# Kernel optimization log

Measured on AMD Instinct MI355X. Metric: run time of the kernel, lower is better.

Reference implementation:

```python
import jax, jax.numpy as jnp
import numpy as np

NUM_HEADS = 8
BN_EPS = 1e-5


def _conv3x3(x, w, B, N, s):
    # x: (B, N, 3*s*s). Torch loops conv2d per batch element; equivalent to one
    # conv over the flattened (B*N, 3, s, s) batch.
    xi = x.reshape(B * N, 3, s, s)
    y = jax.lax.conv_general_dilated(
        xi, w, window_strides=(1, 1), padding='SAME',
        dimension_numbers=('NCHW', 'OIHW', 'NCHW'))
    return y.reshape(B, N, 3 * s * s)


def setup_inputs() -> dict:
    key = jax.random.key(0)
    ks = jax.random.split(key, 8)
    B, N, C, s = 4, 1024, 768, 16
    H = NUM_HEADS
    q = jax.random.normal(ks[0], (B, N, C), jnp.float32)
    k = jax.random.normal(ks[1], (B, N, C), jnp.float32)
    v = jax.random.normal(ks[2], (B, N, C), jnp.float32)
    qw = jax.random.normal(ks[3], (3, 3, 3, 3), jnp.float32) * 0.1
    kw = jax.random.normal(ks[4], (3, 3, 3, 3), jnp.float32) * 0.1
    vw = jax.random.normal(ks[5], (3, 3, 3, 3), jnp.float32) * 0.1
    rw = jax.random.normal(ks[6], (H, H), jnp.float32) * 0.3  # Conv2d(H,H,1,1) weight
    rb = jnp.zeros((H,), jnp.float32)
    bn_gamma = jnp.ones((H,), jnp.float32)
    bn_beta = jnp.zeros((H,), jnp.float32)
    pw = jax.random.normal(ks[7], (C, C), jnp.float32) * 0.02
    pb = jnp.zeros((C,), jnp.float32)
    return dict(q=q, k=k, v=v, qw=qw, kw=kw, vw=vw, rw=rw, rb=rb,
                bn_gamma=bn_gamma, bn_beta=bn_beta, pw=pw, pb=pb)


def reference(q, k, v, qw, kw, vw, rw, rb, bn_gamma, bn_beta, pw, pb):
    B, N, C = q.shape
    H = NUM_HEADS
    d = C // H
    s = int(np.sqrt(C // 3))
    scale = d ** -0.5
    # conv-projected q/k/v, back to (B, N, C)
    qc = _conv3x3(q, qw, B, N, s)
    kc = _conv3x3(k, kw, B, N, s)
    vc = _conv3x3(v, vw, B, N, s)
    # split heads: (B, H, N, d)
    qh = qc.reshape(B, N, H, d).transpose(0, 2, 1, 3)
    kh = kc.reshape(B, N, H, d).transpose(0, 2, 1, 3)
    vh = vc.reshape(B, N, H, d).transpose(0, 2, 1, 3)
    attn = jax.nn.softmax(jnp.einsum('bhnd,bhmd->bhnm', qh, kh) * scale, axis=-1)
    # re-attention: 1x1 cross-head conv + BatchNorm2d(H) in eval mode
    # (running_mean=0, running_var=1); reatten_scale = 1.0
    attn = jnp.einsum('bhnm,gh->bgnm', attn, rw) + rb[None, :, None, None]
    attn = attn * (bn_gamma / jnp.sqrt(1.0 + BN_EPS))[None, :, None, None] \
           + bn_beta[None, :, None, None]
    x = jnp.einsum('bhnm,bhmd->bhnd', attn, vh)
    x = x.transpose(0, 2, 1, 3).reshape(B, N, C)
    return x @ pw.T + pb
```

## Files before the change

### kernel.cpp

```cpp
#include <hip/hip_runtime.h>
#include <hip/hip_bf16.h>
#include <math.h>

#define B 4
#define N 1024
#define C 768
#define H 8
#define D 96

typedef _Float16 half8 __attribute__((ext_vector_type(8)));
typedef _Float16 half4 __attribute__((ext_vector_type(4)));
typedef float f32x4 __attribute__((ext_vector_type(4)));

#define BN_RSQ 0.9999950000374997f
#define QK_SCALE 0.10206207261596577f

__global__ __launch_bounds__(256) void conv_tok(const float* __restrict__ x,
                                                const float* __restrict__ w,
                                                _Float16* __restrict__ out) {
    __shared__ float sx[768];
    __shared__ float sw[81];
    int t = blockIdx.x;
    const float* xt = x + (size_t)t * 768;
    int tid = threadIdx.x;
    sx[tid]       = xt[tid];
    sx[tid + 256] = xt[tid + 256];
    sx[tid + 512] = xt[tid + 512];
    if (tid < 81) sw[tid] = w[tid];
    __syncthreads();
    int i = tid >> 4, j = tid & 15;
    float acc0 = 0.f, acc1 = 0.f, acc2 = 0.f;
    #pragma unroll
    for (int c = 0; c < 3; ++c) {
        #pragma unroll
        for (int di = 0; di < 3; ++di) {
            int ii = i + di - 1;
            if (ii < 0 || ii > 15) continue;
            #pragma unroll
            for (int dj = 0; dj < 3; ++dj) {
                int jj = j + dj - 1;
                if (jj < 0 || jj > 15) continue;
                float xv = sx[c * 256 + ii * 16 + jj];
                acc0 += xv * sw[(0 * 3 + c) * 9 + di * 3 + dj];
                acc1 += xv * sw[(1 * 3 + c) * 9 + di * 3 + dj];
                acc2 += xv * sw[(2 * 3 + c) * 9 + di * 3 + dj];
            }
        }
    }
    _Float16* ot = out + (size_t)t * 768;
    ot[0 * 256 + tid] = (_Float16)acc0;
    ot[1 * 256 + tid] = (_Float16)acc1;
    ot[2 * 256 + tid] = (_Float16)acc2;
}

__global__ __launch_bounds__(256) void transpose_v(const _Float16* __restrict__ vcH,
                                                   _Float16* __restrict__ vcT) {
    __shared__ _Float16 tile[64][66];
    int n0 = blockIdx.x * 64, c0 = blockIdx.y * 64, b = blockIdx.z;
    int tid = threadIdx.x;
    for (int i = tid; i < 4096; i += 256) {
        int r = i >> 6, c = i & 63;
        tile[r][c] = vcH[((size_t)(b * N + n0 + r)) * C + c0 + c];
    }
    __syncthreads();
    for (int i = tid; i < 4096; i += 256) {
        int cr = i >> 6, nc = i & 63;
        vcT[((size_t)(b * 768 + c0 + cr)) * N + n0 + nc] = tile[nc][cr];
    }
}

__global__ __launch_bounds__(256) void vsum_row(const _Float16* __restrict__ vcT,
                                                float* __restrict__ vsum) {
    int row = blockIdx.x * 4 + (threadIdx.x >> 6);
    int lane = threadIdx.x & 63;
    const _Float16* p = vcT + (size_t)row * N;
    float s = 0.f;
    #pragma unroll
    for (int it = 0; it < 2; ++it) {
        half8 v = *(const half8*)(p + (it * 64 + lane) * 8);
        #pragma unroll
        for (int i = 0; i < 8; ++i) s += (float)v[i];
    }
    #pragma unroll
    for (int off = 1; off < 64; off <<= 1) s += __shfl_xor(s, off);
    if (lane == 0) vsum[row] = s;
}

__global__ __launch_bounds__(256) void qk_mfma(const _Float16* __restrict__ qcH,
                                               const _Float16* __restrict__ kcH,
                                               _Float16* __restrict__ expS,
                                               float* __restrict__ Lrow) {
    __shared__ __align__(16) char smem[49152];
    char* Qb = smem;
    char* Kb = smem + 24576;
    const int n0 = blockIdx.x * 128, m0 = blockIdx.y * 128, z = blockIdx.z;
    const int b = z >> 3, h = z & 7;
    const int tid = threadIdx.x;
    const _Float16* qg = qcH + ((size_t)(b * N + n0)) * C + h * D;
    const _Float16* kg = kcH + ((size_t)(b * N + m0)) * C + h * D;
    #pragma unroll
    for (int it = 0; it < 6; ++it) {
        int chunk = it * 256 + tid;
        int r = chunk / 12, cc = (chunk - r * 12) * 8;
        half8 qv = *(const half8*)(qg + (size_t)r * C + cc);
        half8 kv = *(const half8*)(kg + (size_t)r * C + cc);
        int off = ((r * 96 + cc) * 2) ^ ((r & 7) << 4);
        *(half8*)(Qb + off) = qv;
        *(half8*)(Kb + off) = kv;
    }
    __syncthreads();
    const int wid = tid >> 6, lane = tid & 63;
    const int wr = wid >> 1, wc = wid & 1;
    const int l15 = lane & 15, l4 = lane >> 4;
    f32x4 acc[4][4] = {};
    #pragma unroll
    for (int ks = 0; ks < 3; ++ks) {
        int k0 = ks * 32 + l4 * 8;
        half8 a[4], bf[4];
        #pragma unroll
        for (int fm = 0; fm < 4; ++fm) {
            int row = wr * 64 + fm * 16 + l15;
            a[fm] = *(half8*)(Qb + (((row * 96 + k0) * 2) ^ ((row & 7) << 4)));
        }
        #pragma unroll
        for (int fn = 0; fn < 4; ++fn) {
            int row = wc * 64 + fn * 16 + l15;
            bf[fn] = *(half8*)(Kb + (((row * 96 + k0) * 2) ^ ((row & 7) << 4)));
        }
        #pragma unroll
        for (int fm = 0; fm < 4; ++fm)
            #pragma unroll
            for (int fn = 0; fn < 4; ++fn)
                acc[fm][fn] = __builtin_amdgcn_mfma_f32_16x16x32_f16(a[fm], bf[fn], acc[fm][fn], 0, 0, 0);
    }
    __syncthreads();
    #pragma unroll
    for (int fm = 0; fm < 4; ++fm) {
        #pragma unroll
        for (int j = 0; j < 4; ++j) {
            int row = wr * 64 + fm * 16 + l4 * 4 + j;
            float rs = 0.f;
            #pragma unroll
            for (int fn = 0; fn < 4; ++fn) {
                float p = __expf(acc[fm][fn][j] * QK_SCALE);
                rs += p;
                int col = wc * 64 + fn * 16 + l15;
                *(_Float16*)(smem + (row * 136 + col) * 2) = (_Float16)p;
            }
            rs += __shfl_xor(rs, 1);
            rs += __shfl_xor(rs, 2);
            rs += __shfl_xor(rs, 4);
            rs += __shfl_xor(rs, 8);
            if (l15 == 0) atomicAdd(&Lrow[z * N + n0 + row], rs);
        }
    }
    __syncthreads();
    _Float16* eg = expS + ((size_t)z * N + n0) * N + m0;
    #pragma unroll
    for (int it = 0; it < 8; ++it) {
        int q2 = it * 256 + tid;
        int row = q2 >> 4, col8 = (q2 & 15) * 8;
        half8 v = *(half8*)(smem + (row * 136 + col8) * 2);
        *(half8*)(eg + (size_t)row * N + col8) = v;
    }
}

__global__ __launch_bounds__(512, 2) void pv_fused(const _Float16* __restrict__ expS,
                                                   const float* __restrict__ Lrow,
                                                   const _Float16* __restrict__ vcT,
                                                   const float* __restrict__ rw,
                                                   const float* __restrict__ gamma,
                                                   float* __restrict__ x) {
    __shared__ _Float16 AL[8 * 64 * 32];
    __shared__ float w2s[64];
    const int n0 = blockIdx.x * 64;
    const int mbase = blockIdx.y * 256;
    const int b = blockIdx.z;
    const int tid = threadIdx.x;
    if (tid < 64) {
        int g = tid >> 3, hh = tid & 7;
        w2s[tid] = gamma[g] * BN_RSQ * rw[g * 8 + hh];
    }
    const int n_t = tid >> 3;
    const int mq = (tid & 7) * 4;
    float IL[8];
    #pragma unroll
    for (int h = 0; h < 8; ++h)
        IL[h] = 1.0f / Lrow[(size_t)(b * 8 + h) * N + n0 + n_t];
    __syncthreads();
    const int wid = tid >> 6, lane = tid & 63;
    const int l15 = lane & 15, l4 = lane >> 4;
    char* ALb = (char*)AL;
    const _Float16* vgbase = vcT + (size_t)(b * 768 + wid * 96) * N;
    f32x4 acc[4][6] = {};
    for (int msub = 0; msub < 8; ++msub) {
        const int m0 = mbase + msub * 32;
        half4 sE[8];
        #pragma unroll
        for (int h = 0; h < 8; ++h)
            sE[h] = *(const half4*)(expS + ((size_t)(b * 8 + h) * N + n0 + n_t) * N + m0 + mq);
        f32x4 Pq[8];
        #pragma unroll
        for (int h = 0; h < 8; ++h) {
            #pragma unroll
            for (int i = 0; i < 4; ++i) Pq[h][i] = (float)sE[h][i] * IL[h];
        }
        __syncthreads();
        #pragma unroll
        for (int g = 0; g < 8; ++g) {
            f32x4 v = {};
            #pragma unroll
            for (int h = 0; h < 8; ++h) {
                float wv = w2s[g * 8 + h];
                #pragma unroll
                for (int i = 0; i < 4; ++i) v[i] += wv * Pq[h][i];
            }
            half4 hv;
            #pragma unroll
            for (int i = 0; i < 4; ++i) hv[i] = (_Float16)v[i];
            *(half4*)(ALb + (g * 4096 + (((n_t * 32 + mq) * 2) ^ ((n_t & 7) << 4)))) = hv;
        }
        __syncthreads();
        half8 af[4];
        #pragma unroll
        for (int fm = 0; fm < 4; ++fm) {
            int n = fm * 16 + l15;
            af[fm] = *(half8*)(ALb + wid * 4096 + (((n * 32 + l4 * 8) * 2) ^ ((n & 7) << 4)));
        }
        #pragma unroll
        for (int fn = 0; fn < 6; ++fn) {
            int d = fn * 16 + l15;
            half8 bf = *(const half8*)(vgbase + (size_t)d * N + m0 + l4 * 8);
            #pragma unroll
            for (int fm = 0; fm < 4; ++fm)
                acc[fm][fn] = __builtin_amdgcn_mfma_f32_16x16x32_f16(af[fm], bf, acc[fm][fn], 0, 0, 0);
        }
    }
    #pragma unroll
    for (int fm = 0; fm < 4; ++fm)
        #pragma unroll
        for (int fn = 0; fn < 6; ++fn)
            #pragma unroll
            for (int j = 0; j < 4; ++j) {
                int n = n0 + fm * 16 + l4 * 4 + j;
                int c = wid * 96 + fn * 16 + l15;
                atomicAdd(&x[((size_t)(b * N + n)) * C + c], acc[fm][fn][j]);
            }
}

__global__ __launch_bounds__(256) void proj_mfma(const float* __restrict__ x,
                                                 const float* __restrict__ vsum,
                                                 const float* __restrict__ pw,
                                                 const float* __restrict__ pb,
                                                 const float* __restrict__ rb,
                                                 const float* __restrict__ gamma,
                                                 const float* __restrict__ beta,
                                                 float* __restrict__ out) {
    __shared__ _Float16 sX[128 * 32];
    __shared__ _Float16 sW[96 * 32];
    const int t0 = blockIdx.x * 128, c0 = blockIdx.y * 96;
    const int b = t0 >> 10;
    const int tid = threadIdx.x;
    const int wid = tid >> 6, lane = tid & 63;
    const int wr = wid >> 1, wc = wid & 1;
    const int l15 = lane & 15, l4 = lane >> 4;
    char* Xb = (char*)sX;
    char* Wb = (char*)sW;
    f32x4 acc[4][3] = {};
    for (int k0 = 0; k0 < 768; k0 += 32) {
        __syncthreads();
        #pragma unroll
        for (int it = 0; it < 4; ++it) {
            int q = it * 256 + tid;
            int r = q >> 3, c4 = (q & 7) * 4;
            f32x4 xv = *(const f32x4*)(x + (size_t)(t0 + r) * C + k0 + c4);
            int g = (k0 + c4) / 96;
            float cg = gamma[g] * BN_RSQ * rb[g] + beta[g];
            const f32x4 vs = *(const f32x4*)(vsum + b * 768 + k0 + c4);
            half4 hv;
            #pragma unroll
            for (int i = 0; i < 4; ++i) hv[i] = (_Float16)(xv[i] + cg * vs[i]);
            *(half4*)(Xb + (((r * 32 + c4) * 2) ^ ((r & 7) << 4))) = hv;
        }
        #pragma unroll
        for (int it = 0; it < 3; ++it) {
            int q = it * 256 + tid;
            int r = q >> 3, c4 = (q & 7) * 4;
            f32x4 wv = *(const f32x4*)(pw + (size_t)(c0 + r) * C + k0 + c4);
            half4 hv;
            #pragma unroll
            for (int i = 0; i < 4; ++i) hv[i] = (_Float16)wv[i];
            *(half4*)(Wb + (((r * 32 + c4) * 2) ^ ((r & 7) << 4))) = hv;
        }
        __syncthreads();
        half8 af[4];
        #pragma unroll
        for (int fm = 0; fm < 4; ++fm) {
            int r = wr * 64 + fm * 16 + l15;
            af[fm] = *(half8*)(Xb + (((r * 32 + l4 * 8) * 2) ^ ((r & 7) << 4)));
        }
        #pragma unroll
        for (int fn = 0; fn < 3; ++fn) {
            int r = wc * 48 + fn * 16 + l15;
            half8 bf = *(half8*)(Wb + (((r * 32 + l4 * 8) * 2) ^ ((r & 7) << 4)));
            #pragma unroll
            for (int fm = 0; fm < 4; ++fm)
                acc[fm][fn] = __builtin_amdgcn_mfma_f32_16x16x32_f16(af[fm], bf, acc[fm][fn], 0, 0, 0);
        }
    }
    #pragma unroll
    for (int fm = 0; fm < 4; ++fm)
        #pragma unroll
        for (int fn = 0; fn < 3; ++fn) {
            int cc = c0 + wc * 48 + fn * 16 + l15;
            float bias = pb[cc];
            #pragma unroll
            for (int j = 0; j < 4; ++j) {
                int t = t0 + wr * 64 + fm * 16 + l4 * 4 + j;
                out[(size_t)t * C + cc] = acc[fm][fn][j] + bias;
            }
        }
}

extern "C" void kernel_launch(void* const* d_in, const int* in_sizes, int n_in,
                              void* d_out, int out_size, void* d_ws, size_t ws_size,
                              hipStream_t stream) {
    const float* q     = (const float*)d_in[0];
    const float* k     = (const float*)d_in[1];
    const float* v     = (const float*)d_in[2];
    const float* qw    = (const float*)d_in[3];
    const float* kw    = (const float*)d_in[4];
    const float* vw    = (const float*)d_in[5];
    const float* rw    = (const float*)d_in[6];
    const float* rb    = (const float*)d_in[7];
    const float* gamma = (const float*)d_in[8];
    const float* beta  = (const float*)d_in[9];
    const float* pw    = (const float*)d_in[10];
    const float* pb    = (const float*)d_in[11];
    float* out = (float*)d_out;

    char* ws = (char*)d_ws;
    _Float16* expS = (_Float16*)ws;
    float*    xacc = (float*)(ws + 67108864);
    _Float16* qcH  = (_Float16*)(ws + 79691776);
    _Float16* kcH  = (_Float16*)(ws + 85983232);
    _Float16* vcH  = (_Float16*)(ws + 92274688);
    _Float16* vcT  = (_Float16*)(ws + 98566144);
    float*    Lrow = (float*)(ws + 104857600);
    float*    vsum = (float*)(ws + 104988672);

    hipMemsetAsync(Lrow, 0, 131072, stream);
    hipMemsetAsync(xacc, 0, 12582912, stream);

    conv_tok<<<dim3(B * N), dim3(256), 0, stream>>>(q, qw, qcH);
    conv_tok<<<dim3(B * N), dim3(256), 0, stream>>>(k, kw, kcH);
    conv_tok<<<dim3(B * N), dim3(256), 0, stream>>>(v, vw, vcH);

    transpose_v<<<dim3(16, 12, B), dim3(256), 0, stream>>>(vcH, vcT);
    vsum_row<<<dim3(768), dim3(256), 0, stream>>>(vcT, vsum);

    qk_mfma<<<dim3(8, 8, 8 * B), dim3(256), 0, stream>>>(qcH, kcH, expS, Lrow);

    pv_fused<<<dim3(16, 4, B), dim3(512), 0, stream>>>(expS, Lrow, vcT, rw, gamma, xacc);

    proj_mfma<<<dim3(32, 8), dim3(256), 0, stream>>>(xacc, vsum, pw, pb, rb, gamma, beta, out);
}
```

Before: 262.4 us.

## Recompute QK^T in PV kernel instead of materializing exp scores

```diff
diff --git a/kernel.cpp b/kernel.cpp
--- a/kernel.cpp
+++ b/kernel.cpp
@@ -86,165 +86,197 @@
     if (lane == 0) vsum[row] = s;
 }
 
-__global__ __launch_bounds__(256) void qk_mfma(const _Float16* __restrict__ qcH,
-                                               const _Float16* __restrict__ kcH,
-                                               _Float16* __restrict__ expS,
-                                               float* __restrict__ Lrow) {
+__global__ __launch_bounds__(256) void lrow_mfma(const _Float16* __restrict__ qcH,
+                                                 const _Float16* __restrict__ kcH,
+                                                 float* __restrict__ Lrow) {
     __shared__ __align__(16) char smem[49152];
     char* Qb = smem;
     char* Kb = smem + 24576;
-    const int n0 = blockIdx.x * 128, m0 = blockIdx.y * 128, z = blockIdx.z;
+    const int n0 = blockIdx.x * 128, z = blockIdx.y;
     const int b = z >> 3, h = z & 7;
     const int tid = threadIdx.x;
     const _Float16* qg = qcH + ((size_t)(b * N + n0)) * C + h * D;
-    const _Float16* kg = kcH + ((size_t)(b * N + m0)) * C + h * D;
+    const _Float16* kgb = kcH + ((size_t)(b * N)) * C + h * D;
     #pragma unroll
     for (int it = 0; it < 6; ++it) {
         int chunk = it * 256 + tid;
         int r = chunk / 12, cc = (chunk - r * 12) * 8;
         half8 qv = *(const half8*)(qg + (size_t)r * C + cc);
-        half8 kv = *(const half8*)(kg + (size_t)r * C + cc);
-        int off = ((r * 96 + cc) * 2) ^ ((r & 7) << 4);
-        *(half8*)(Qb + off) = qv;
-        *(half8*)(Kb + off) = kv;
-    }
-    __syncthreads();
+        *(half8*)(Qb + (((r * 96 + cc) * 2) ^ ((r & 7) << 4))) = qv;
+    }
     const int wid = tid >> 6, lane = tid & 63;
     const int wr = wid >> 1, wc = wid & 1;
     const int l15 = lane & 15, l4 = lane >> 4;
-    f32x4 acc[4][4] = {};
-    #pragma unroll
-    for (int ks = 0; ks < 3; ++ks) {
-        int k0 = ks * 32 + l4 * 8;
-        half8 a[4], bf[4];
-        #pragma unroll
-        for (int fm = 0; fm < 4; ++fm) {
-            int row = wr * 64 + fm * 16 + l15;
-            a[fm] = *(half8*)(Qb + (((row * 96 + k0) * 2) ^ ((row & 7) << 4)));
-        }
-        #pragma unroll
-        for (int fn = 0; fn < 4; ++fn) {
-            int row = wc * 64 + fn * 16 + l15;
-            bf[fn] = *(half8*)(Kb + (((row * 96 + k0) * 2) ^ ((row & 7) << 4)));
+    float rs[4][4] = {};
+    for (int m0 = 0; m0 < 1024; m0 += 128) {
+        __syncthreads();
+        #pragma unroll
+        for (int it = 0; it < 6; ++it) {
+            int chunk = it * 256 + tid;
+            int r = chunk / 12, cc = (chunk - r * 12) * 8;
+            half8 kv = *(const half8*)(kgb + (size_t)(m0 + r) * C + cc);
+            *(half8*)(Kb + (((r * 96 + cc) * 2) ^ ((r & 7) << 4))) = kv;
+        }
+        __syncthreads();
+        f32x4 acc[4][4] = {};
+        #pragma unroll
+        for (int ks = 0; ks < 3; ++ks) {
+            int k0 = ks * 32 + l4 * 8;
+            half8 a[4], bf[4];
+            #pragma unroll
+            for (int fm = 0; fm < 4; ++fm) {
+                int row = wr * 64 + fm * 16 + l15;
+                a[fm] = *(half8*)(Qb + (((row * 96 + k0) * 2) ^ ((row & 7) << 4)));
+            }
+            #pragma unroll
+            for (int fn = 0; fn < 4; ++fn) {
+                int row = wc * 64 + fn * 16 + l15;
+                bf[fn] = *(half8*)(Kb + (((row * 96 + k0) * 2) ^ ((row & 7) << 4)));
+            }
+            #pragma unroll
+            for (int fm = 0; fm < 4; ++fm)
+                #pragma unroll
+                for (int fn = 0; fn < 4; ++fn)
+                    acc[fm][fn] = __builtin_amdgcn_mfma_f32_16x16x32_f16(a[fm], bf[fn], acc[fm][fn], 0, 0, 0);
         }
         #pragma unroll
         for (int fm = 0; fm < 4; ++fm)
             #pragma unroll
-            for (int fn = 0; fn < 4; ++fn)
-                acc[fm][fn] = __builtin_amdgcn_mfma_f32_16x16x32_f16(a[fm], bf[fn], acc[fm][fn], 0, 0, 0);
-    }
-    __syncthreads();
-    #pragma unroll
-    for (int fm = 0; fm < 4; ++fm) {
+            for (int j = 0; j < 4; ++j) {
+                float s = 0.f;
+                #pragma unroll
+                for (int fn = 0; fn < 4; ++fn)
+                    s += __expf(acc[fm][fn][j] * QK_SCALE);
+                rs[fm][j] += s;
+            }
+    }
+    #pragma unroll
+    for (int fm = 0; fm < 4; ++fm)
         #pragma unroll
         for (int j = 0; j < 4; ++j) {
-            int row = wr * 64 + fm * 16 + l4 * 4 + j;
-            float rs = 0.f;
-            #pragma unroll
-            for (int fn = 0; fn < 4; ++fn) {
-                float p = __expf(acc[fm][fn][j] * QK_SCALE);
-                rs += p;
-                int col = wc * 64 + fn * 16 + l15;
-                *(_Float16*)(smem + (row * 136 + col) * 2) = (_Float16)p;
-            }
-            rs += __shfl_xor(rs, 1);
-            rs += __shfl_xor(rs, 2);
-            rs += __shfl_xor(rs, 4);
-            rs += __shfl_xor(rs, 8);
-            if (l15 == 0) atomicAdd(&Lrow[z * N + n0 + row], rs);
-        }
-    }
-    __syncthreads();
-    _Float16* eg = expS + ((size_t)z * N + n0) * N + m0;
-    #pragma unroll
-    for (int it = 0; it < 8; ++it) {
-        int q2 = it * 256 + tid;
-        int row = q2 >> 4, col8 = (q2 & 15) * 8;
-        half8 v = *(half8*)(smem + (row * 136 + col8) * 2);
-        *(half8*)(eg + (size_t)row * N + col8) = v;
-    }
-}
-
-__global__ __launch_bounds__(512, 2) void pv_fused(const _Float16* __restrict__ expS,
-                                                   const float* __restrict__ Lrow,
-                                                   const _Float16* __restrict__ vcT,
-                                                   const float* __restrict__ rw,
-                                                   const float* __restrict__ gamma,
-                                                   float* __restrict__ x) {
-    __shared__ _Float16 AL[8 * 64 * 32];
+            float s = rs[fm][j];
+            s += __shfl_xor(s, 1);
+            s += __shfl_xor(s, 2);
+            s += __shfl_xor(s, 4);
+            s += __shfl_xor(s, 8);
+            if (l15 == 0)
+                atomicAdd(&Lrow[z * N + n0 + wr * 64 + fm * 16 + l4 * 4 + j], s);
+        }
+}
+
+__global__ __launch_bounds__(512) void mixpv(const _Float16* __restrict__ qcH,
+                                             const _Float16* __restrict__ kcH,
+                                             const _Float16* __restrict__ vcT,
+                                             const float* __restrict__ Lrow,
+                                             const float* __restrict__ rw,
+                                             const float* __restrict__ gamma,
+                                             float* __restrict__ x) {
+    __shared__ __align__(16) _Float16 P[8 * 32 * 64];
     __shared__ float w2s[64];
-    const int n0 = blockIdx.x * 64;
-    const int mbase = blockIdx.y * 256;
+    const int n0 = blockIdx.x * 32;
+    const int msbase = blockIdx.y * 512;
     const int b = blockIdx.z;
     const int tid = threadIdx.x;
     if (tid < 64) {
         int g = tid >> 3, hh = tid & 7;
         w2s[tid] = gamma[g] * BN_RSQ * rw[g * 8 + hh];
     }
-    const int n_t = tid >> 3;
-    const int mq = (tid & 7) * 4;
+    const int n_t = tid >> 4;
+    const int mq4 = (tid & 15) * 4;
     float IL[8];
     #pragma unroll
     for (int h = 0; h < 8; ++h)
         IL[h] = 1.0f / Lrow[(size_t)(b * 8 + h) * N + n0 + n_t];
-    __syncthreads();
     const int wid = tid >> 6, lane = tid & 63;
     const int l15 = lane & 15, l4 = lane >> 4;
-    char* ALb = (char*)AL;
-    const _Float16* vgbase = vcT + (size_t)(b * 768 + wid * 96) * N;
-    f32x4 acc[4][6] = {};
-    for (int msub = 0; msub < 8; ++msub) {
-        const int m0 = mbase + msub * 32;
-        half4 sE[8];
-        #pragma unroll
-        for (int h = 0; h < 8; ++h)
-            sE[h] = *(const half4*)(expS + ((size_t)(b * 8 + h) * N + n0 + n_t) * N + m0 + mq);
-        f32x4 Pq[8];
-        #pragma unroll
-        for (int h = 0; h < 8; ++h) {
-            #pragma unroll
-            for (int i = 0; i < 4; ++i) Pq[h][i] = (float)sE[h][i] * IL[h];
-        }
-        __syncthreads();
-        #pragma unroll
-        for (int g = 0; g < 8; ++g) {
-            f32x4 v = {};
+    char* Pb = (char*)P;
+    half8 q8[2][3];
+    #pragma unroll
+    for (int fm = 0; fm < 2; ++fm)
+        #pragma unroll
+        for (int ks = 0; ks < 3; ++ks)
+            q8[fm][ks] = *(const half8*)(qcH + (size_t)(b * N + n0 + fm * 16 + l15) * C
+                                         + wid * 96 + ks * 32 + l4 * 8);
+    __syncthreads();
+    f32x4 acc_u[2][6] = {};
+    for (int mt = 0; mt < 8; ++mt) {
+        const int m0 = msbase + mt * 64;
+        #pragma unroll
+        for (int fn = 0; fn < 4; ++fn) {
+            half8 kf[3];
+            #pragma unroll
+            for (int ks = 0; ks < 3; ++ks)
+                kf[ks] = *(const half8*)(kcH + (size_t)(b * N + m0 + fn * 16 + l15) * C
+                                         + wid * 96 + ks * 32 + l4 * 8);
+            f32x4 a4[2] = {};
+            #pragma unroll
+            for (int ks = 0; ks < 3; ++ks)
+                #pragma unroll
+                for (int fm = 0; fm < 2; ++fm)
+                    a4[fm] = __builtin_amdgcn_mfma_f32_16x16x32_f16(q8[fm][ks], kf[ks], a4[fm], 0, 0, 0);
+            #pragma unroll
+            for (int fm = 0; fm < 2; ++fm)
+                #pragma unroll
+                for (int j = 0; j < 4; ++j) {
+                    float p = __expf(a4[fm][j] * QK_SCALE);
+                    int n = fm * 16 + l4 * 4 + j;
+                    int m = fn * 16 + l15;
+                    *(_Float16*)(Pb + wid * 4096 + ((n * 128 + m * 2) ^ ((n & 7) << 4))) = (_Float16)p;
+                }
+        }
+        __syncthreads();
+        {
+            f32x4 vmix[8] = {};
             #pragma unroll
             for (int h = 0; h < 8; ++h) {
-                float wv = w2s[g * 8 + h];
-                #pragma unroll
-                for (int i = 0; i < 4; ++i) v[i] += wv * Pq[h][i];
-            }
-            half4 hv;
-            #pragma unroll
-            for (int i = 0; i < 4; ++i) hv[i] = (_Float16)v[i];
-            *(half4*)(ALb + (g * 4096 + (((n_t * 32 + mq) * 2) ^ ((n_t & 7) << 4)))) = hv;
-        }
-        __syncthreads();
-        half8 af[4];
-        #pragma unroll
-        for (int fm = 0; fm < 4; ++fm) {
-            int n = fm * 16 + l15;
-            af[fm] = *(half8*)(ALb + wid * 4096 + (((n * 32 + l4 * 8) * 2) ^ ((n & 7) << 4)));
-        }
-        #pragma unroll
-        for (int fn = 0; fn < 6; ++fn) {
-            int d = fn * 16 + l15;
-            half8 bf = *(const half8*)(vgbase + (size_t)d * N + m0 + l4 * 8);
-            #pragma unroll
-            for (int fm = 0; fm < 4; ++fm)
-                acc[fm][fn] = __builtin_amdgcn_mfma_f32_16x16x32_f16(af[fm], bf, acc[fm][fn], 0, 0, 0);
-        }
-    }
-    #pragma unroll
-    for (int fm = 0; fm < 4; ++fm)
-        #pragma unroll
-        for (int fn = 0; fn < 6; ++fn)
+                half4 p4 = *(half4*)(Pb + h * 4096 + ((n_t * 128 + mq4 * 2) ^ ((n_t & 7) << 4)));
+                f32x4 pq;
+                #pragma unroll
+                for (int i = 0; i < 4; ++i) pq[i] = (float)p4[i] * IL[h];
+                #pragma unroll
+                for (int g = 0; g < 8; ++g) {
+                    float wv = w2s[g * 8 + h];
+                    #pragma unroll
+                    for (int i = 0; i < 4; ++i) vmix[g][i] += wv * pq[i];
+                }
+            }
+            #pragma unroll
+            for (int g = 0; g < 8; ++g) {
+                half4 hv;
+                #pragma unroll
+                for (int i = 0; i < 4; ++i) hv[i] = (_Float16)vmix[g][i];
+                *(half4*)(Pb + g * 4096 + ((n_t * 128 + mq4 * 2) ^ ((n_t & 7) << 4))) = hv;
+            }
+        }
+        __syncthreads();
+        #pragma unroll
+        for (int ks2 = 0; ks2 < 2; ++ks2) {
+            half8 af[2];
+            #pragma unroll
+            for (int fm = 0; fm < 2; ++fm) {
+                int n = fm * 16 + l15;
+                af[fm] = *(half8*)(Pb + wid * 4096 + ((n * 128 + (ks2 * 32 + l4 * 8) * 2) ^ ((n & 7) << 4)));
+            }
+            #pragma unroll
+            for (int fn2 = 0; fn2 < 6; ++fn2) {
+                half8 vf = *(const half8*)(vcT + (size_t)(b * 768 + wid * 96 + fn2 * 16 + l15) * N
+                                           + m0 + ks2 * 32 + l4 * 8);
+                #pragma unroll
+                for (int fm = 0; fm < 2; ++fm)
+                    acc_u[fm][fn2] = __builtin_amdgcn_mfma_f32_16x16x32_f16(af[fm], vf, acc_u[fm][fn2], 0, 0, 0);
+            }
+        }
+        __syncthreads();
+    }
+    #pragma unroll
+    for (int fm = 0; fm < 2; ++fm)
+        #pragma unroll
+        for (int fn2 = 0; fn2 < 6; ++fn2)
             #pragma unroll
             for (int j = 0; j < 4; ++j) {
                 int n = n0 + fm * 16 + l4 * 4 + j;
-                int c = wid * 96 + fn * 16 + l15;
-                atomicAdd(&x[((size_t)(b * N + n)) * C + c], acc[fm][fn][j]);
+                int c = wid * 96 + fn2 * 16 + l15;
+                atomicAdd(&x[((size_t)(b * N + n)) * C + c], acc_u[fm][fn2][j]);
             }
 }
 
@@ -340,14 +372,13 @@
     float* out = (float*)d_out;
 
     char* ws = (char*)d_ws;
-    _Float16* expS = (_Float16*)ws;
-    float*    xacc = (float*)(ws + 67108864);
-    _Float16* qcH  = (_Float16*)(ws + 79691776);
-    _Float16* kcH  = (_Float16*)(ws + 85983232);
-    _Float16* vcH  = (_Float16*)(ws + 92274688);
-    _Float16* vcT  = (_Float16*)(ws + 98566144);
-    float*    Lrow = (float*)(ws + 104857600);
-    float*    vsum = (float*)(ws + 104988672);
+    float*    xacc = (float*)ws;
+    _Float16* qcH  = (_Float16*)(ws + 12582912);
+    _Float16* kcH  = (_Float16*)(ws + 18874368);
+    _Float16* vcH  = (_Float16*)(ws + 25165824);
+    _Float16* vcT  = (_Float16*)(ws + 31457280);
+    float*    Lrow = (float*)(ws + 37748736);
+    float*    vsum = (float*)(ws + 37879808);
 
     hipMemsetAsync(Lrow, 0, 131072, stream);
     hipMemsetAsync(xacc, 0, 12582912, stream);
@@ -359,9 +390,9 @@
     transpose_v<<<dim3(16, 12, B), dim3(256), 0, stream>>>(vcH, vcT);
     vsum_row<<<dim3(768), dim3(256), 0, stream>>>(vcT, vsum);
 
-    qk_mfma<<<dim3(8, 8, 8 * B), dim3(256), 0, stream>>>(qcH, kcH, expS, Lrow);
-
-    pv_fused<<<dim3(16, 4, B), dim3(512), 0, stream>>>(expS, Lrow, vcT, rw, gamma, xacc);
+    lrow_mfma<<<dim3(8, 32), dim3(256), 0, stream>>>(qcH, kcH, Lrow);
+
+    mixpv<<<dim3(32, 2, B), dim3(512), 0, stream>>>(qcH, kcH, vcT, Lrow, rw, gamma, xacc);
 
     proj_mfma<<<dim3(32, 8), dim3(256), 0, stream>>>(xacc, vsum, pw, pb, rb, gamma, beta, out);
 }
```

Measured after the change: 273.7 us. 1.04x slower.

## Rewrite PV kernel as LDS-free register head-mixing with XCD-aware tiling; merge convs

Applied to the files above, without the earlier changes.

```diff
diff --git a/kernel.cpp b/kernel.cpp
--- a/kernel.cpp
+++ b/kernel.cpp
@@ -10,14 +10,39 @@
 
 typedef _Float16 half8 __attribute__((ext_vector_type(8)));
 typedef _Float16 half4 __attribute__((ext_vector_type(4)));
+typedef _Float16 h2 __attribute__((ext_vector_type(2)));
 typedef float f32x4 __attribute__((ext_vector_type(4)));
 
 #define BN_RSQ 0.9999950000374997f
 #define QK_SCALE 0.10206207261596577f
 
-__global__ __launch_bounds__(256) void conv_tok(const float* __restrict__ x,
-                                                const float* __restrict__ w,
-                                                _Float16* __restrict__ out) {
+static __device__ __forceinline__ h2 u32_to_h2(unsigned int u) {
+    union { unsigned int u; h2 h; } c; c.u = u; return c.h;
+}
+
+__global__ __launch_bounds__(64) void w2prep(const float* __restrict__ rw,
+                                             const float* __restrict__ gamma,
+                                             unsigned int* __restrict__ w2pk) {
+    int t = threadIdx.x;
+    int g = t >> 3, h = t & 7;
+    float w = gamma[g] * BN_RSQ * rw[g * 8 + h];
+    union { _Float16 f; unsigned short s; } c; c.f = (_Float16)w;
+    w2pk[t] = (unsigned int)c.s | ((unsigned int)c.s << 16);
+}
+
+__global__ __launch_bounds__(256) void conv_all(const float* __restrict__ q,
+                                                const float* __restrict__ k,
+                                                const float* __restrict__ v,
+                                                const float* __restrict__ qw,
+                                                const float* __restrict__ kw,
+                                                const float* __restrict__ vw,
+                                                _Float16* __restrict__ qo,
+                                                _Float16* __restrict__ ko,
+                                                _Float16* __restrict__ vo) {
+    const int sel = blockIdx.y;
+    const float* x = sel == 0 ? q : sel == 1 ? k : v;
+    const float* w = sel == 0 ? qw : sel == 1 ? kw : vw;
+    _Float16* out = sel == 0 ? qo : sel == 1 ? ko : vo;
     __shared__ float sx[768];
     __shared__ float sw[81];
     int t = blockIdx.x;
@@ -165,86 +190,79 @@
     }
 }
 
-__global__ __launch_bounds__(512, 2) void pv_fused(const _Float16* __restrict__ expS,
-                                                   const float* __restrict__ Lrow,
-                                                   const _Float16* __restrict__ vcT,
-                                                   const float* __restrict__ rw,
-                                                   const float* __restrict__ gamma,
-                                                   float* __restrict__ x) {
-    __shared__ _Float16 AL[8 * 64 * 32];
-    __shared__ float w2s[64];
-    const int n0 = blockIdx.x * 64;
-    const int mbase = blockIdx.y * 256;
-    const int b = blockIdx.z;
+__global__ __launch_bounds__(256) void pv3(const _Float16* __restrict__ expS,
+                                           const float* __restrict__ Lrow,
+                                           const _Float16* __restrict__ vcT,
+                                           const unsigned int* __restrict__ w2pk,
+                                           float* __restrict__ x) {
+    const int gid = blockIdx.x;
+    const int xcd = gid & 7;
+    const int idx = gid >> 3;
+    const int bmq = xcd * 2 + (idx & 1);
+    const int b = bmq >> 2, mq = bmq & 3;
+    const int n0 = (idx >> 1) * 16;
+    const int mbase = mq * 256;
     const int tid = threadIdx.x;
-    if (tid < 64) {
-        int g = tid >> 3, hh = tid & 7;
-        w2s[tid] = gamma[g] * BN_RSQ * rw[g * 8 + hh];
-    }
-    const int n_t = tid >> 3;
-    const int mq = (tid & 7) * 4;
-    float IL[8];
-    #pragma unroll
-    for (int h = 0; h < 8; ++h)
-        IL[h] = 1.0f / Lrow[(size_t)(b * 8 + h) * N + n0 + n_t];
-    __syncthreads();
-    const int wid = tid >> 6, lane = tid & 63;
+    const int wv = tid >> 6, lane = tid & 63;
     const int l15 = lane & 15, l4 = lane >> 4;
-    char* ALb = (char*)AL;
-    const _Float16* vgbase = vcT + (size_t)(b * 768 + wid * 96) * N;
-    f32x4 acc[4][6] = {};
-    for (int msub = 0; msub < 8; ++msub) {
-        const int m0 = mbase + msub * 32;
-        half4 sE[8];
-        #pragma unroll
-        for (int h = 0; h < 8; ++h)
-            sE[h] = *(const half4*)(expS + ((size_t)(b * 8 + h) * N + n0 + n_t) * N + m0 + mq);
-        f32x4 Pq[8];
-        #pragma unroll
-        for (int h = 0; h < 8; ++h) {
-            #pragma unroll
-            for (int i = 0; i < 4; ++i) Pq[h][i] = (float)sE[h][i] * IL[h];
-        }
-        __syncthreads();
-        #pragma unroll
-        for (int g = 0; g < 8; ++g) {
-            f32x4 v = {};
+    const int g0 = wv * 2;
+    h2 IL2[8];
+    #pragma unroll
+    for (int h = 0; h < 8; ++h) {
+        float il = 1.0f / Lrow[(size_t)(b * 8 + h) * N + n0 + l15];
+        _Float16 i16 = (_Float16)il;
+        h2 t; t[0] = i16; t[1] = i16;
+        IL2[h] = t;
+    }
+    f32x4 acc[2][6] = {};
+    const size_t erow = ((size_t)(b * 8) * N + n0 + l15) * N;
+    const size_t estride = (size_t)N * N;
+    #pragma unroll
+    for (int mt = 0; mt < 4; ++mt) {
+        const int m0 = mbase + mt * 64;
+        #pragma unroll
+        for (int ks2 = 0; ks2 < 2; ++ks2) {
+            const int moff = m0 + ks2 * 32 + l4 * 8;
+            h2 pn[8][4];
             #pragma unroll
             for (int h = 0; h < 8; ++h) {
-                float wv = w2s[g * 8 + h];
+                half8 p8 = *(const half8*)(expS + erow + (size_t)h * estride + moff);
                 #pragma unroll
-                for (int i = 0; i < 4; ++i) v[i] += wv * Pq[h][i];
-            }
-            half4 hv;
-            #pragma unroll
-            for (int i = 0; i < 4; ++i) hv[i] = (_Float16)v[i];
-            *(half4*)(ALb + (g * 4096 + (((n_t * 32 + mq) * 2) ^ ((n_t & 7) << 4)))) = hv;
-        }
-        __syncthreads();
-        half8 af[4];
-        #pragma unroll
-        for (int fm = 0; fm < 4; ++fm) {
-            int n = fm * 16 + l15;
-            af[fm] = *(half8*)(ALb + wid * 4096 + (((n * 32 + l4 * 8) * 2) ^ ((n & 7) << 4)));
-        }
-        #pragma unroll
-        for (int fn = 0; fn < 6; ++fn) {
-            int d = fn * 16 + l15;
-            half8 bf = *(const half8*)(vgbase + (size_t)d * N + m0 + l4 * 8);
-            #pragma unroll
-            for (int fm = 0; fm < 4; ++fm)
-                acc[fm][fn] = __builtin_amdgcn_mfma_f32_16x16x32_f16(af[fm], bf, acc[fm][fn], 0, 0, 0);
-        }
-    }
-    #pragma unroll
-    for (int fm = 0; fm < 4; ++fm)
-        #pragma unroll
-        for (int fn = 0; fn < 6; ++fn)
+                for (int i = 0; i < 4; ++i) {
+                    h2 t; t[0] = p8[2 * i]; t[1] = p8[2 * i + 1];
+                    pn[h][i] = t * IL2[h];
+                }
+            }
+            #pragma unroll
+            for (int gg = 0; gg < 2; ++gg) {
+                const int g = g0 + gg;
+                h2 am[4] = {};
+                #pragma unroll
+                for (int h = 0; h < 8; ++h) {
+                    h2 w = u32_to_h2(w2pk[g * 8 + h]);
+                    #pragma unroll
+                    for (int i = 0; i < 4; ++i) am[i] = w * pn[h][i] + am[i];
+                }
+                half8 af;
+                #pragma unroll
+                for (int i = 0; i < 4; ++i) { af[2 * i] = am[i][0]; af[2 * i + 1] = am[i][1]; }
+                #pragma unroll
+                for (int fn2 = 0; fn2 < 6; ++fn2) {
+                    half8 vf = *(const half8*)(vcT + (size_t)(b * 768 + g * 96 + fn2 * 16 + l15) * N + moff);
+                    acc[gg][fn2] = __builtin_amdgcn_mfma_f32_16x16x32_f16(af, vf, acc[gg][fn2], 0, 0, 0);
+                }
+            }
+        }
+    }
+    #pragma unroll
+    for (int gg = 0; gg < 2; ++gg)
+        #pragma unroll
+        for (int fn2 = 0; fn2 < 6; ++fn2)
             #pragma unroll
             for (int j = 0; j < 4; ++j) {
-                int n = n0 + fm * 16 + l4 * 4 + j;
-                int c = wid * 96 + fn * 16 + l15;
-                atomicAdd(&x[((size_t)(b * N + n)) * C + c], acc[fm][fn][j]);
+                int n = n0 + l4 * 4 + j;
+                int c = (g0 + gg) * 96 + fn2 * 16 + l15;
+                atomicAdd(&x[((size_t)(b * N + n)) * C + c], acc[gg][fn2][j]);
             }
 }
 
@@ -348,20 +366,21 @@
     _Float16* vcT  = (_Float16*)(ws + 98566144);
     float*    Lrow = (float*)(ws + 104857600);
     float*    vsum = (float*)(ws + 104988672);
+    unsigned int* w2pk = (unsigned int*)(ws + 105000960);
 
     hipMemsetAsync(Lrow, 0, 131072, stream);
     hipMemsetAsync(xacc, 0, 12582912, stream);
 
-    conv_tok<<<dim3(B * N), dim3(256), 0, stream>>>(q, qw, qcH);
-    conv_tok<<<dim3(B * N), dim3(256), 0, stream>>>(k, kw, kcH);
-    conv_tok<<<dim3(B * N), dim3(256), 0, stream>>>(v, vw, vcH);
+    w2prep<<<dim3(1), dim3(64), 0, stream>>>(rw, gamma, w2pk);
+
+    conv_all<<<dim3(B * N, 3), dim3(256), 0, stream>>>(q, k, v, qw, kw, vw, qcH, kcH, vcH);
 
     transpose_v<<<dim3(16, 12, B), dim3(256), 0, stream>>>(vcH, vcT);
     vsum_row<<<dim3(768), dim3(256), 0, stream>>>(vcT, vsum);
 
     qk_mfma<<<dim3(8, 8, 8 * B), dim3(256), 0, stream>>>(qcH, kcH, expS, Lrow);
 
-    pv_fused<<<dim3(16, 4, B), dim3(512), 0, stream>>>(expS, Lrow, vcT, rw, gamma, xacc);
+    pv3<<<dim3(1024), dim3(256), 0, stream>>>(expS, Lrow, vcT, w2pk, xacc);
 
     proj_mfma<<<dim3(32, 8), dim3(256), 0, stream>>>(xacc, vsum, pw, pb, rb, gamma, beta, out);
 }
```

Result: slower. 311.5 us (+18.7%).
